# Kernel optimization log

Measured on AMD Instinct MI355X. Metric: run time of the kernel, lower is better.

The kernel has to match this reference:

```python
import jax, jax.numpy as jnp
import numpy as np

MIN_NORM = 1e-15
BALL_EPS = 4e-3  # float32 boundary eps used by the PoincareBall manifold


def _norm(x):
    return jnp.maximum(jnp.linalg.norm(x, axis=-1, keepdims=True), MIN_NORM)


def _artanh(x):
    # clamp like torch Artanh autograd fn (1e-7 margin)
    return jnp.arctanh(jnp.clip(x, -1.0 + 1e-7, 1.0 - 1e-7))


def proj(x, c):
    n = _norm(x)
    maxnorm = (1.0 - BALL_EPS) / jnp.sqrt(c)
    return jnp.where(n > maxnorm, x / n * maxnorm, x)


def expmap0(u, c):
    sc = jnp.sqrt(c)
    n = _norm(u)
    return jnp.tanh(sc * n) * u / (sc * n)


def logmap0(p, c):
    sc = jnp.sqrt(c)
    n = _norm(p)
    return _artanh(sc * n) * p / (sc * n)


def mobius_add(x, y, c):
    x2 = jnp.sum(x * x, axis=-1, keepdims=True)
    y2 = jnp.sum(y * y, axis=-1, keepdims=True)
    xy = jnp.sum(x * y, axis=-1, keepdims=True)
    num = (1.0 + 2.0 * c * xy + c * y2) * x + (1.0 - c * x2) * y
    denom = 1.0 + 2.0 * c * xy + c * c * x2 * y2
    return num / jnp.maximum(denom, MIN_NORM)


def mobius_matvec(m, x, c):
    sc = jnp.sqrt(c)
    xn = _norm(x)
    mx = x @ m.T  # [N, out]
    mxn = _norm(mx)
    res = jnp.tanh(mxn / xn * _artanh(sc * xn)) * mx / (mxn * sc)
    is_zero = jnp.all(mx == 0, axis=-1, keepdims=True)
    return jnp.where(is_zero, jnp.zeros_like(res), res)


def setup_inputs() -> dict:
    key = jax.random.key(0)
    N, D_IN, D_OUT, E = 100000, 128, 128, 1600000
    k1, k2, k3, k4, k5 = jax.random.split(key, 5)
    # points inside the Poincare ball (||x|| ~ 0.34 < 1)
    x = 0.03 * jax.random.normal(k1, (N, D_IN), dtype=jnp.float32)
    # xavier_uniform with gain sqrt(2)
    limit = np.sqrt(2.0) * np.sqrt(6.0 / (D_IN + D_OUT))
    weight = jax.random.uniform(k2, (D_OUT, D_IN), minval=-limit, maxval=limit, dtype=jnp.float32)
    bias = jnp.zeros((D_OUT,), dtype=jnp.float32)
    edge_index = jax.random.randint(k3, (2, E), 0, N, dtype=jnp.int64)
    edge_weight = jax.random.uniform(k4, (E,), dtype=jnp.float32) / 16.0
    return {"x": x, "weight": weight, "bias": bias,
            "edge_index": edge_index, "edge_weight": edge_weight,
            "num_nodes": N}


def reference(x, weight, bias, edge_index, edge_weight, num_nodes):
    c_in = 1.0
    c_out = 1.0
    # --- OriginHypLinear (dropout=0 / eval) ---
    mv = proj(mobius_matvec(weight, x, c_in), c_in)
    hyp_bias = proj(expmap0(bias[None, :], c_in), c_in)  # proj_tan0 is identity
    h = proj(mobius_add(mv, hyp_bias, c_in), c_in)
    # --- OriginHypAgg: logmap0 -> spmm -> expmap0 ---
    xt = logmap0(h, c_in)
    dst, src = edge_index[0], edge_index[1]
    support = jax.ops.segment_sum(edge_weight[:, None] * xt[src], dst,
                                  num_segments=num_nodes)
    h = proj(expmap0(support, c_in), c_in)
    # --- OriginHypAct: relu in tangent space ---
    xt = jax.nn.relu(logmap0(h, c_in))  # proj_tan0 identity
    return proj(expmap0(xt, c_out), c_out)
```

## Files before the change

kernel.cpp:

```cpp
#include <hip/hip_runtime.h>
#include <math.h>

#define D 128
#define MAXNORM 0.996f
#define MINNORM 1e-15f
#define ATCLAMP (1.0f - 1e-7f)

#define CHUNK 2048
#define BSH   7
#define MAXNB 1024
#define SCAP  6144

typedef unsigned int   u32;
typedef unsigned short u16;

typedef __attribute__((ext_vector_type(8))) short bf16x8;
typedef __attribute__((ext_vector_type(4))) float f32x4;

__device__ __forceinline__ float wsum(float v) {
#pragma unroll
  for (int m = 32; m; m >>= 1) v += __shfl_xor(v, m);
  return v;
}
__device__ __forceinline__ float rsum16(float v) {
#pragma unroll
  for (int m = 1; m <= 8; m <<= 1) v += __shfl_xor(v, m);
  return v;
}

__device__ __forceinline__ float frcp(float x) { return __builtin_amdgcn_rcpf(x); }

__device__ __forceinline__ float fast_artanh(float x) {
  x = fminf(x, ATCLAMP);
  return 0.5f * __logf((1.0f + x) * frcp(1.0f - x));
}
__device__ __forceinline__ float fast_tanh(float z) {
  float t = __expf(-2.0f * z);
  return (1.0f - t) * frcp(1.0f + t);
}

__device__ __forceinline__ float bflo(u32 u) { return __uint_as_float(u << 16); }
__device__ __forceinline__ float bfhi(u32 u) { return __uint_as_float(u & 0xffff0000u); }
__device__ __forceinline__ u16 f2bf(float f) {
  u32 u = __float_as_uint(f);
  return (u16)((u + 0x7fffu + ((u >> 16) & 1u)) >> 16);
}
__device__ __forceinline__ float bf2f(u16 h) { return __uint_as_float(((u32)h) << 16); }

union U4B8 { uint4 u; bf16x8 b; };
__device__ __forceinline__ bf16x8 as_b8(uint4 v) { U4B8 c; c.u = v; return c.b; }

__device__ __forceinline__ bool detect_bf16(const u32* p) {
  float lo = fabsf(bflo(p[threadIdx.x & 63]));
  return (bool)__all(lo < 1.0f);
}
__device__ __forceinline__ bool detect_i64(const int* p) {
  return (bool)__all(p[2 * (threadIdx.x & 63) + 1] == 0);
}

template<bool BF>
__device__ __forceinline__ void k1_body(const void* xv, const void* Wv,
                                        const void* bv, u16* xt, int N,
                                        uint4* Wh, uint4* Wl) {
  const int tid  = threadIdx.x;
  const int lane = tid & 63;
  const int wid  = tid >> 6;
  const int qg   = lane >> 4;
  const int lc   = lane & 15;

  for (int slot = tid; slot < 2048; slot += 256) {
    const int l = slot & 63, frag = slot >> 6;
    const int t = frag >> 2, ks = frag & 3;
    const int j  = (l & 15) + 16 * t;
    const int k0 = 32 * ks + 8 * (l >> 4);
    if (BF) {
      Wh[slot] = ((const uint4*)Wv)[j * 16 + (k0 >> 3)];
    } else {
      const float* Wf = (const float*)Wv;
      float4 f0 = *(const float4*)(Wf + (size_t)j * D + k0);
      float4 f1 = *(const float4*)(Wf + (size_t)j * D + k0 + 4);
      float f[8] = {f0.x, f0.y, f0.z, f0.w, f1.x, f1.y, f1.z, f1.w};
      u32 hw[4], lw[4];
#pragma unroll
      for (int i = 0; i < 4; ++i) {
        u16 h0 = f2bf(f[2*i]),  h1 = f2bf(f[2*i+1]);
        u16 l0 = f2bf(f[2*i]   - bf2f(h0));
        u16 l1 = f2bf(f[2*i+1] - bf2f(h1));
        hw[i] = (u32)h0 | ((u32)h1 << 16);
        lw[i] = (u32)l0 | ((u32)l1 << 16);
      }
      Wh[slot] = make_uint4(hw[0], hw[1], hw[2], hw[3]);
      Wl[slot] = make_uint4(lw[0], lw[1], lw[2], lw[3]);
    }
  }

  float bfr[8];
  float nb2 = 0.f;
#pragma unroll
  for (int t = 0; t < 8; ++t) {
    float v = BF ? bf2f(((const u16*)bv)[lc + 16 * t])
                 : ((const float*)bv)[lc + 16 * t];
    bfr[t] = v; nb2 += v * v;
  }
  nb2 = rsum16(nb2);
  float y2;
  {
    float nb = fmaxf(sqrtf(nb2), MINNORM);
    float s  = fast_tanh(nb) * frcp(nb);
    float n1 = s * nb;
    if (n1 > MAXNORM) s *= MAXNORM * frcp(n1);
#pragma unroll
    for (int t = 0; t < 8; ++t) bfr[t] *= s;
    y2 = s * s * nb2;
  }
  const bool bias_zero = (y2 == 0.0f);

  __syncthreads();

  const int tile  = blockIdx.x * 4 + wid;
  const int rbase = tile * 16;
  if (rbase >= N) return;

  int rowA = rbase + lc; if (rowA >= N) rowA = N - 1;
  uint4 Ah[4], Al[4];
  float xn2 = 0.f;
  if (BF) {
    const uint4* xr = (const uint4*)((const u16*)xv + (size_t)rowA * D);
#pragma unroll
    for (int ks = 0; ks < 4; ++ks) {
      uint4 v = xr[4 * ks + qg];
      Ah[ks] = v;
      float a0 = bflo(v.x), a1 = bfhi(v.x), a2 = bflo(v.y), a3 = bfhi(v.y);
      float a4 = bflo(v.z), a5 = bfhi(v.z), a6 = bflo(v.w), a7 = bfhi(v.w);
      xn2 += a0*a0 + a1*a1 + a2*a2 + a3*a3 + a4*a4 + a5*a5 + a6*a6 + a7*a7;
    }
  } else {
    const float4* xr = (const float4*)((const float*)xv + (size_t)rowA * D);
#pragma unroll
    for (int ks = 0; ks < 4; ++ks) {
      float4 f0 = xr[8 * ks + 2 * qg], f1 = xr[8 * ks + 2 * qg + 1];
      float f[8] = {f0.x, f0.y, f0.z, f0.w, f1.x, f1.y, f1.z, f1.w};
      u32 hw[4], lw[4];
#pragma unroll
      for (int i = 0; i < 4; ++i) {
        u16 h0 = f2bf(f[2*i]),  h1 = f2bf(f[2*i+1]);
        u16 l0 = f2bf(f[2*i]   - bf2f(h0));
        u16 l1 = f2bf(f[2*i+1] - bf2f(h1));
        hw[i] = (u32)h0 | ((u32)h1 << 16);
        lw[i] = (u32)l0 | ((u32)l1 << 16);
        xn2 += f[2*i] * f[2*i] + f[2*i+1] * f[2*i+1];
      }
      Ah[ks] = make_uint4(hw[0], hw[1], hw[2], hw[3]);
      Al[ks] = make_uint4(lw[0], lw[1], lw[2], lw[3]);
    }
  }
  xn2 += __shfl_xor(xn2, 16);
  xn2 += __shfl_xor(xn2, 32);

  f32x4 acc[8];
  const f32x4 zero = {0.f, 0.f, 0.f, 0.f};
#pragma unroll
  for (int t = 0; t < 8; ++t) acc[t] = zero;
#pragma unroll
  for (int ks = 0; ks < 4; ++ks) {
    bf16x8 a = as_b8(Ah[ks]);
    bf16x8 al;
    if (!BF) al = as_b8(Al[ks]);
#pragma unroll
    for (int t = 0; t < 8; ++t) {
      const int idx = (t * 4 + ks) * 64 + lane;
      bf16x8 bh = as_b8(Wh[idx]);
      acc[t] = __builtin_amdgcn_mfma_f32_16x16x32_bf16(a, bh, acc[t], 0, 0, 0);
      if (!BF) {
        bf16x8 bl = as_b8(Wl[idx]);
        acc[t] = __builtin_amdgcn_mfma_f32_16x16x32_bf16(al, bh, acc[t], 0, 0, 0);
        acc[t] = __builtin_amdgcn_mfma_f32_16x16x32_bf16(a,  bl, acc[t], 0, 0, 0);
      }
    }
  }

#pragma unroll
  for (int q = 0; q < 4; ++q) {
    const int row_off = qg * 4 + q;
    const int row = rbase + row_off;
    float xnq = fmaxf(sqrtf(__shfl(xn2, row_off)), MINNORM);
    float s2 = 0.f;
#pragma unroll
    for (int t = 0; t < 8; ++t) { float v = acc[t][q]; s2 += v * v; }
    s2 = rsum16(s2);
    float mxn = fmaxf(sqrtf(s2), MINNORM);
    float r = fast_tanh(mxn * frcp(xnq) * fast_artanh(xnq)) * frcp(mxn);
    float pn = r * mxn;
    if (pn > MAXNORM) { r *= MAXNORM * frcp(pn); pn = MAXNORM; }
    float h[8];
    float hn;
    if (bias_zero) {
#pragma unroll
      for (int t = 0; t < 8; ++t) h[t] = r * acc[t][q];
      hn = pn;
    } else {
      float xy = 0.f;
#pragma unroll
      for (int t = 0; t < 8; ++t) { h[t] = r * acc[t][q]; xy += h[t] * bfr[t]; }
      xy = rsum16(xy);
      float x2 = pn * pn;
      float ca = 1.f + 2.f * xy + y2;
      float cb = 1.f - x2;
      float id = frcp(fmaxf(1.f + 2.f * xy + x2 * y2, MINNORM));
      float s3 = 0.f;
#pragma unroll
      for (int t = 0; t < 8; ++t) { h[t] = (ca * h[t] + cb * bfr[t]) * id; s3 += h[t] * h[t]; }
      hn = fmaxf(sqrtf(rsum16(s3)), MINNORM);
    }
    float ps = (hn > MAXNORM) ? (MAXNORM * frcp(hn)) : 1.f;
    float np = fmaxf(hn * ps, MINNORM);
    float tsc = fast_artanh(np) * frcp(np) * ps;
    if (row < N) {
      u16* xo = xt + (size_t)row * D + lc;
#pragma unroll
      for (int t = 0; t < 8; ++t) xo[16 * t] = f2bf(tsc * h[t]);
    }
  }
}

extern "C" __global__ __launch_bounds__(256)
void OriginHyperbolicGraphConvolution_38628935860614_kernel(
    const void* x, const void* W, const void* b, u16* xt, int N) {
  __shared__ uint4 Wh[2048];
  __shared__ uint4 Wl[2048];
  if (detect_bf16((const u32*)x)) k1_body<true >(x, W, b, xt, N, Wh, Wl);
  else                            k1_body<false>(x, W, b, xt, N, Wh, Wl);
}

extern "C" __global__ __launch_bounds__(256) void ksA(
    const int* ei, const void* ew, uint2* ebuck, u16* soffs, int E, int N, int nb) {
  __shared__ int   hist[MAXNB];
  __shared__ int   sArr[MAXNB + 1];
  __shared__ int   psum[256];
  __shared__ uint2 recs[CHUNK];
  const bool i64 = detect_i64(ei);
  const bool bf  = detect_bf16((const u32*)ew);
  const int tid   = threadIdx.x;
  const int cbase = blockIdx.x * CHUNK;

  for (int i = tid; i < MAXNB; i += 256) hist[i] = 0;
  __syncthreads();

  int bkt[8], rank[8]; u32 px[8], wb[8]; bool val[8];
#pragma unroll
  for (int r = 0; r < 8; ++r) {
    const int e = cbase + r * 256 + tid;
    val[r] = false;
    if (e < E) {
      int dst, src;
      if (i64) { dst = ei[2 * (size_t)e]; src = ei[2 * ((size_t)E + e)]; }
      else     { dst = ei[e];             src = ei[(size_t)E + e]; }
      if ((unsigned)dst < (unsigned)N && (unsigned)src < (unsigned)N) {
        val[r] = true;
        bkt[r] = dst >> BSH;
        px[r]  = (u32)src | ((u32)(dst & ((1 << BSH) - 1)) << 17);
        float w;
        if (bf) w = bf2f(((const u16*)ew)[e]); else w = ((const float*)ew)[e];
        wb[r] = __float_as_uint(w);
        rank[r] = atomicAdd(&hist[bkt[r]], 1);
      }
    }
  }
  __syncthreads();

  const int g0 = tid * 4;
  int loc[4], ts = 0;
#pragma unroll
  for (int i = 0; i < 4; ++i) { loc[i] = ts; ts += hist[g0 + i]; }
  psum[tid] = ts; __syncthreads();
#pragma unroll
  for (int off = 1; off < 256; off <<= 1) {
    int t = (tid >= off) ? psum[tid - off] : 0;
    __syncthreads();
    psum[tid] += t;
    __syncthreads();
  }
  const int excl = psum[tid] - ts;
#pragma unroll
  for (int i = 0; i < 4; ++i) sArr[g0 + i] = excl + loc[i];
  if (tid == 255) sArr[MAXNB] = psum[255];
  __syncthreads();

#pragma unroll
  for (int r = 0; r < 8; ++r) if (val[r])
    recs[sArr[bkt[r]] + rank[r]] = make_uint2(px[r], wb[r]);
  __syncthreads();

  const int vcnt = sArr[MAXNB];
  for (int i = tid; i < vcnt; i += 256) ebuck[(size_t)cbase + i] = recs[i];
  u16* so = soffs + (size_t)blockIdx.x * (nb + 1);
  for (int b = tid; b <= nb; b += 256) so[b] = (u16)sArr[b];
}

extern "C" __global__ __launch_bounds__(256) void ks2sum(
    const u16* soffs, int* btot, int nb, int nchunks) {
  __shared__ int red[256];
  const int b = blockIdx.x, tid = threadIdx.x;
  int s = 0;
  for (int c = tid; c < nchunks; c += 256) {
    const u16* so = soffs + (size_t)c * (nb + 1) + b;
    s += (int)so[1] - (int)so[0];
  }
  red[tid] = s; __syncthreads();
#pragma unroll
  for (int off = 128; off; off >>= 1) {
    if (tid < off) red[tid] += red[tid + off];
    __syncthreads();
  }
  if (tid == 0) btot[b] = red[0];
}

extern "C" __global__ __launch_bounds__(1024) void ks2scan(
    const int* btot, int* bbase, int nb) {
  __shared__ int sc[1024];
  const int t = threadIdx.x;
  int v = (t < nb) ? btot[t] : 0;
  sc[t] = v; __syncthreads();
#pragma unroll
  for (int off = 1; off < 1024; off <<= 1) {
    int u = (t >= off) ? sc[t - off] : 0;
    __syncthreads();
    sc[t] += u;
    __syncthreads();
  }
  if (t < nb) bbase[t] = sc[t] - v;
  if (t == 1023) bbase[nb] = sc[1023];
}

extern "C" __global__ __launch_bounds__(256) void ks3(
    const uint2* ebuck, const u16* soffs, const int* bbase,
    uint2* esrt, int* offs, int N, int nb, int nchunks) {
  __shared__ uint2 stage[SCAP];
  __shared__ int hist[128], sc[128], cur[128];
  __shared__ int lcur;
  const int tid = threadIdx.x;
  const int b = blockIdx.x;
  const int s0 = bbase[b], s1 = bbase[b + 1], sz = s1 - s0;
  if (tid < 128) hist[tid] = 0;
  if (tid == 0) lcur = 0;
  __syncthreads();

  const bool fit = (sz <= SCAP);
  if (fit) {
    for (int c = tid; c < nchunks; c += 256) {
      const u16* so = soffs + (size_t)c * (nb + 1) + b;
      const int a = so[0], e = so[1];
      if (e > a) {
        const int base = atomicAdd(&lcur, e - a);
        for (int j = a; j < e; ++j) {
          const uint2 r = ebuck[(size_t)c * CHUNK + j];
          stage[base + (j - a)] = r;
          atomicAdd(&hist[(r.x >> 17) & 127], 1);
        }
      }
    }
  } else {
    for (int c = tid; c < nchunks; c += 256) {
      const u16* so = soffs + (size_t)c * (nb + 1) + b;
      for (int j = so[0]; j < so[1]; ++j)
        atomicAdd(&hist[(ebuck[(size_t)c * CHUNK + j].x >> 17) & 127], 1);
    }
  }
  __syncthreads();

  int v = 0;
  if (tid < 128) { v = hist[tid]; sc[tid] = v; }
  __syncthreads();
#pragma unroll
  for (int off = 1; off < 128; off <<= 1) {
    int t = (tid < 128 && tid >= off) ? sc[tid - off] : 0;
    __syncthreads();
    if (tid < 128) sc[tid] += t;
    __syncthreads();
  }
  if (tid < 128) {
    const int st = sc[tid] - v;
    cur[tid] = st;
    const int node = (b << BSH) + tid;
    if (node < N) offs[node] = s0 + st;
  }
  if (tid == 0 && b == nb - 1) offs[N] = s1;
  __syncthreads();

  if (fit) {
    for (int i = tid; i < sz; i += 256) {
      const uint2 r = stage[i];
      const int d = atomicAdd(&cur[(r.x >> 17) & 127], 1);
      esrt[s0 + d] = make_uint2(r.x & 0x1FFFFu, r.y);
    }
  } else {
    for (int c = tid; c < nchunks; c += 256) {
      const u16* so = soffs + (size_t)c * (nb + 1) + b;
      for (int j = so[0]; j < so[1]; ++j) {
        const uint2 r = ebuck[(size_t)c * CHUNK + j];
        const int d = atomicAdd(&cur[(r.x >> 17) & 127], 1);
        esrt[s0 + d] = make_uint2(r.x & 0x1FFFFu, r.y);
      }
    }
  }
}

extern "C" __global__ __launch_bounds__(256) void kagg(
    const int* offs, const uint2* esrt, const u16* xt,
    void* out, const void* xdet, int N) {
  const bool bf = detect_bf16((const u32*)xdet);
  const int lane = threadIdx.x & 63;
  const int node = blockIdx.x * 4 + (threadIdx.x >> 6);
  if (node >= N) return;
  int s0 = __builtin_amdgcn_readfirstlane(offs[node]);
  int s1 = __builtin_amdgcn_readfirstlane(offs[node + 1]);
  const uint2* ep = esrt + s0;
  const int cnt = s1 - s0;
  const u32* xtw = (const u32*)xt;
  float a0 = 0.f, a1 = 0.f;
  int i = 0;
  for (; i + 8 <= cnt; i += 8) {
    uint2 e[8]; u32 u[8];
#pragma unroll
    for (int k = 0; k < 8; ++k) e[k] = ep[i + k];
#pragma unroll
    for (int k = 0; k < 8; ++k) u[k] = xtw[(e[k].x << 6) | lane];
#pragma unroll
    for (int k = 0; k < 8; ++k) {
      const float w = __uint_as_float(e[k].y);
      a0 += w * bflo(u[k]);
      a1 += w * bfhi(u[k]);
    }
  }
  for (; i + 4 <= cnt; i += 4) {
    uint2 e[4]; u32 u[4];
#pragma unroll
    for (int k = 0; k < 4; ++k) e[k] = ep[i + k];
#pragma unroll
    for (int k = 0; k < 4; ++k) u[k] = xtw[(e[k].x << 6) | lane];
#pragma unroll
    for (int k = 0; k < 4; ++k) {
      const float w = __uint_as_float(e[k].y);
      a0 += w * bflo(u[k]);
      a1 += w * bfhi(u[k]);
    }
  }
  for (; i < cnt; ++i) {
    const uint2 e = ep[i];
    const u32 u = xtw[(e.x << 6) | lane];
    const float w = __uint_as_float(e.y);
    a0 += w * bflo(u);
    a1 += w * bfhi(u);
  }
  float n = fmaxf(sqrtf(wsum(a0 * a0 + a1 * a1)), MINNORM);
  float tn = fast_tanh(n);
  float m = tn * frcp(n);
  if (tn > MAXNORM) { m *= MAXNORM * frcp(tn); tn = MAXNORM; }
  float nn = fmaxf(tn, MINNORM);
  m *= fast_artanh(nn) * frcp(nn);
  float tA = fmaxf(m * a0, 0.f), tB = fmaxf(m * a1, 0.f);
  float nr = fmaxf(sqrtf(wsum(tA * tA + tB * tB)), MINNORM);
  float t2 = fast_tanh(nr);
  float m2 = t2 * frcp(nr);
  if (t2 > MAXNORM) m2 *= MAXNORM * frcp(t2);
  float oA = m2 * tA, oB = m2 * tB;
  if (bf) {
    u32 o = ((u32)f2bf(oA)) | (((u32)f2bf(oB)) << 16);
    ((u32*)out)[(size_t)node * 64 + lane] = o;
  } else {
    ((float2*)out)[(size_t)node * 64 + lane] = make_float2(oA, oB);
  }
}

extern "C" void kernel_launch(void* const* d_in, const int* in_sizes, int n_in,
                              void* d_out, int out_size, void* d_ws, size_t ws_size,
                              hipStream_t stream) {
  const void* x    = d_in[0];
  const void* W    = d_in[1];
  const void* bias = d_in[2];
  const int*  ei   = (const int*)d_in[3];
  const void* ew   = d_in[4];
  const int N = in_sizes[0] / D;
  const int E = in_sizes[4];
  const int nchunks = (E + CHUNK - 1) / CHUNK;
  const int nb      = (N + (1 << BSH) - 1) >> BSH;

  char* ws = (char*)d_ws;
  size_t off = 0;
  auto carve = [&](size_t bytes) { char* p = ws + off; off = (off + bytes + 255) & ~(size_t)255; return p; };
  u16*   xt     = (u16*)  carve((size_t)N * D * sizeof(u16));
  uint2* ebuck  = (uint2*)carve((size_t)nchunks * CHUNK * sizeof(uint2));
  uint2* esrt   = (uint2*)carve((size_t)E * sizeof(uint2));
  u16*   soffs  = (u16*)  carve((size_t)nchunks * (nb + 1) * sizeof(u16));
  int*   btot   = (int*)  carve((size_t)nb * sizeof(int));
  int*   bbase  = (int*)  carve((size_t)(nb + 1) * sizeof(int));
  int*   offs   = (int*)  carve((size_t)(N + 1) * sizeof(int));

  OriginHyperbolicGraphConvolution_38628935860614_kernel<<<(N + 63) / 64, 256, 0, stream>>>(
      x, W, bias, xt, N);
  ksA   <<<nchunks, 256, 0, stream>>>(ei, ew, ebuck, soffs, E, N, nb);
  ks2sum<<<nb, 256, 0, stream>>>(soffs, btot, nb, nchunks);
  ks2scan<<<1, 1024, 0, stream>>>(btot, bbase, nb);
  ks3   <<<nb, 256, 0, stream>>>(ebuck, soffs, bbase, esrt, offs, N, nb, nchunks);
  kagg  <<<(N + 3) / 4, 256, 0, stream>>>(offs, esrt, xt, d_out, x, N);
}
```

Before: 271.4 us.

## Switch GEMM to single fp16 MFMA, fuse bucket scans, persist tiles, widen gather

The split-bf16 three-MFMA product is replaced by a single fp16 MFMA, and the intermediate tangent features are stored as fp16. The two scan kernels are removed: bucket totals are accumulated atomically in ksA, and each ks3 block computes its own prefix, with offsets stored as (start,count) pairs. The linear kernel becomes a persistent grid-stride loop with occupancy hints and also zeroes the counters. The aggregation loop is unrolled to 16 edges. Together these cut launches, LDS use and MFMA work, at the cost of fp16 range and precision risk and a redundant per-block prefix sum.

Measured after the change: 310.8 us. 1.15x slower.

```diff
diff --git a/kernel.cpp b/kernel.cpp
--- a/kernel.cpp
+++ b/kernel.cpp
@@ -9,12 +9,13 @@
 #define CHUNK 2048
 #define BSH   7
 #define MAXNB 1024
-#define SCAP  6144
+#define SCAP2 5120
 
 typedef unsigned int   u32;
 typedef unsigned short u16;
 
-typedef __attribute__((ext_vector_type(8))) short bf16x8;
+typedef __attribute__((ext_vector_type(8))) _Float16 f16x8;
+typedef __attribute__((ext_vector_type(2))) __fp16   h2raw;
 typedef __attribute__((ext_vector_type(4))) float f32x4;
 
 __device__ __forceinline__ float wsum(float v) {
@@ -41,14 +42,18 @@
 
 __device__ __forceinline__ float bflo(u32 u) { return __uint_as_float(u << 16); }
 __device__ __forceinline__ float bfhi(u32 u) { return __uint_as_float(u & 0xffff0000u); }
-__device__ __forceinline__ u16 f2bf(float f) {
-  u32 u = __float_as_uint(f);
-  return (u16)((u + 0x7fffu + ((u >> 16) & 1u)) >> 16);
-}
 __device__ __forceinline__ float bf2f(u16 h) { return __uint_as_float(((u32)h) << 16); }
 
-union U4B8 { uint4 u; bf16x8 b; };
-__device__ __forceinline__ bf16x8 as_b8(uint4 v) { U4B8 c; c.u = v; return c.b; }
+union H2U { h2raw h; u32 u; };
+__device__ __forceinline__ u32 pkh(float a, float b) {
+  H2U c; c.h = __builtin_amdgcn_cvt_pkrtz(a, b); return c.u;
+}
+union U2H { u32 u; _Float16 h[2]; };
+union U4H8 { uint4 u; f16x8 h; };
+__device__ __forceinline__ f16x8 as_h8(uint4 v) { U4H8 c; c.u = v; return c.h; }
+__device__ __forceinline__ u16 f2h(float f) {
+  _Float16 h = (_Float16)f; return *(u16*)&h;
+}
 
 __device__ __forceinline__ bool detect_bf16(const u32* p) {
   float lo = fabsf(bflo(p[threadIdx.x & 63]));
@@ -61,7 +66,7 @@
 template<bool BF>
 __device__ __forceinline__ void k1_body(const void* xv, const void* Wv,
                                         const void* bv, u16* xt, int N,
-                                        uint4* Wh, uint4* Wl) {
+                                        uint4* Wh) {
   const int tid  = threadIdx.x;
   const int lane = tid & 63;
   const int wid  = tid >> 6;
@@ -73,25 +78,20 @@
     const int t = frag >> 2, ks = frag & 3;
     const int j  = (l & 15) + 16 * t;
     const int k0 = 32 * ks + 8 * (l >> 4);
+    float f[8];
     if (BF) {
-      Wh[slot] = ((const uint4*)Wv)[j * 16 + (k0 >> 3)];
+      uint4 v = ((const uint4*)Wv)[j * 16 + (k0 >> 3)];
+      f[0] = bflo(v.x); f[1] = bfhi(v.x); f[2] = bflo(v.y); f[3] = bfhi(v.y);
+      f[4] = bflo(v.z); f[5] = bfhi(v.z); f[6] = bflo(v.w); f[7] = bfhi(v.w);
     } else {
       const float* Wf = (const float*)Wv;
       float4 f0 = *(const float4*)(Wf + (size_t)j * D + k0);
       float4 f1 = *(const float4*)(Wf + (size_t)j * D + k0 + 4);
-      float f[8] = {f0.x, f0.y, f0.z, f0.w, f1.x, f1.y, f1.z, f1.w};
-      u32 hw[4], lw[4];
-#pragma unroll
-      for (int i = 0; i < 4; ++i) {
-        u16 h0 = f2bf(f[2*i]),  h1 = f2bf(f[2*i+1]);
-        u16 l0 = f2bf(f[2*i]   - bf2f(h0));
-        u16 l1 = f2bf(f[2*i+1] - bf2f(h1));
-        hw[i] = (u32)h0 | ((u32)h1 << 16);
-        lw[i] = (u32)l0 | ((u32)l1 << 16);
-      }
-      Wh[slot] = make_uint4(hw[0], hw[1], hw[2], hw[3]);
-      Wl[slot] = make_uint4(lw[0], lw[1], lw[2], lw[3]);
-    }
+      f[0]=f0.x; f[1]=f0.y; f[2]=f0.z; f[3]=f0.w;
+      f[4]=f1.x; f[5]=f1.y; f[6]=f1.z; f[7]=f1.w;
+    }
+    Wh[slot] = make_uint4(pkh(f[0],f[1]), pkh(f[2],f[3]),
+                          pkh(f[4],f[5]), pkh(f[6],f[7]));
   }
 
   float bfr[8];
@@ -117,123 +117,105 @@
 
   __syncthreads();
 
-  const int tile  = blockIdx.x * 4 + wid;
-  const int rbase = tile * 16;
-  if (rbase >= N) return;
-
-  int rowA = rbase + lc; if (rowA >= N) rowA = N - 1;
-  uint4 Ah[4], Al[4];
-  float xn2 = 0.f;
-  if (BF) {
-    const uint4* xr = (const uint4*)((const u16*)xv + (size_t)rowA * D);
+  const int T = (N + 15) >> 4;
+  for (int tile = blockIdx.x * 4 + wid; tile < T; tile += gridDim.x * 4) {
+    const int rbase = tile * 16;
+    int rowA = rbase + lc; if (rowA >= N) rowA = N - 1;
+    uint4 Ah[4];
+    float xn2 = 0.f;
 #pragma unroll
     for (int ks = 0; ks < 4; ++ks) {
-      uint4 v = xr[4 * ks + qg];
-      Ah[ks] = v;
-      float a0 = bflo(v.x), a1 = bfhi(v.x), a2 = bflo(v.y), a3 = bfhi(v.y);
-      float a4 = bflo(v.z), a5 = bfhi(v.z), a6 = bflo(v.w), a7 = bfhi(v.w);
-      xn2 += a0*a0 + a1*a1 + a2*a2 + a3*a3 + a4*a4 + a5*a5 + a6*a6 + a7*a7;
-    }
-  } else {
-    const float4* xr = (const float4*)((const float*)xv + (size_t)rowA * D);
+      float f[8];
+      if (BF) {
+        uint4 v = ((const uint4*)((const u16*)xv + (size_t)rowA * D))[4 * ks + qg];
+        f[0]=bflo(v.x); f[1]=bfhi(v.x); f[2]=bflo(v.y); f[3]=bfhi(v.y);
+        f[4]=bflo(v.z); f[5]=bfhi(v.z); f[6]=bflo(v.w); f[7]=bfhi(v.w);
+      } else {
+        const float4* xr = (const float4*)((const float*)xv + (size_t)rowA * D);
+        float4 f0 = xr[8 * ks + 2 * qg], f1 = xr[8 * ks + 2 * qg + 1];
+        f[0]=f0.x; f[1]=f0.y; f[2]=f0.z; f[3]=f0.w;
+        f[4]=f1.x; f[5]=f1.y; f[6]=f1.z; f[7]=f1.w;
+      }
+#pragma unroll
+      for (int i = 0; i < 8; ++i) xn2 += f[i] * f[i];
+      Ah[ks] = make_uint4(pkh(f[0],f[1]), pkh(f[2],f[3]),
+                          pkh(f[4],f[5]), pkh(f[6],f[7]));
+    }
+    xn2 += __shfl_xor(xn2, 16);
+    xn2 += __shfl_xor(xn2, 32);
+
+    f32x4 acc[8];
+    const f32x4 zero = {0.f, 0.f, 0.f, 0.f};
+#pragma unroll
+    for (int t = 0; t < 8; ++t) acc[t] = zero;
 #pragma unroll
     for (int ks = 0; ks < 4; ++ks) {
-      float4 f0 = xr[8 * ks + 2 * qg], f1 = xr[8 * ks + 2 * qg + 1];
-      float f[8] = {f0.x, f0.y, f0.z, f0.w, f1.x, f1.y, f1.z, f1.w};
-      u32 hw[4], lw[4];
-#pragma unroll
-      for (int i = 0; i < 4; ++i) {
-        u16 h0 = f2bf(f[2*i]),  h1 = f2bf(f[2*i+1]);
-        u16 l0 = f2bf(f[2*i]   - bf2f(h0));
-        u16 l1 = f2bf(f[2*i+1] - bf2f(h1));
-        hw[i] = (u32)h0 | ((u32)h1 << 16);
-        lw[i] = (u32)l0 | ((u32)l1 << 16);
-        xn2 += f[2*i] * f[2*i] + f[2*i+1] * f[2*i+1];
-      }
-      Ah[ks] = make_uint4(hw[0], hw[1], hw[2], hw[3]);
-      Al[ks] = make_uint4(lw[0], lw[1], lw[2], lw[3]);
-    }
-  }
-  xn2 += __shfl_xor(xn2, 16);
-  xn2 += __shfl_xor(xn2, 32);
-
-  f32x4 acc[8];
-  const f32x4 zero = {0.f, 0.f, 0.f, 0.f};
-#pragma unroll
-  for (int t = 0; t < 8; ++t) acc[t] = zero;
-#pragma unroll
-  for (int ks = 0; ks < 4; ++ks) {
-    bf16x8 a = as_b8(Ah[ks]);
-    bf16x8 al;
-    if (!BF) al = as_b8(Al[ks]);
-#pragma unroll
-    for (int t = 0; t < 8; ++t) {
-      const int idx = (t * 4 + ks) * 64 + lane;
-      bf16x8 bh = as_b8(Wh[idx]);
-      acc[t] = __builtin_amdgcn_mfma_f32_16x16x32_bf16(a, bh, acc[t], 0, 0, 0);
-      if (!BF) {
-        bf16x8 bl = as_b8(Wl[idx]);
-        acc[t] = __builtin_amdgcn_mfma_f32_16x16x32_bf16(al, bh, acc[t], 0, 0, 0);
-        acc[t] = __builtin_amdgcn_mfma_f32_16x16x32_bf16(a,  bl, acc[t], 0, 0, 0);
-      }
-    }
-  }
-
-#pragma unroll
-  for (int q = 0; q < 4; ++q) {
-    const int row_off = qg * 4 + q;
-    const int row = rbase + row_off;
-    float xnq = fmaxf(sqrtf(__shfl(xn2, row_off)), MINNORM);
-    float s2 = 0.f;
-#pragma unroll
-    for (int t = 0; t < 8; ++t) { float v = acc[t][q]; s2 += v * v; }
-    s2 = rsum16(s2);
-    float mxn = fmaxf(sqrtf(s2), MINNORM);
-    float r = fast_tanh(mxn * frcp(xnq) * fast_artanh(xnq)) * frcp(mxn);
-    float pn = r * mxn;
-    if (pn > MAXNORM) { r *= MAXNORM * frcp(pn); pn = MAXNORM; }
-    float h[8];
-    float hn;
-    if (bias_zero) {
-#pragma unroll
-      for (int t = 0; t < 8; ++t) h[t] = r * acc[t][q];
-      hn = pn;
-    } else {
-      float xy = 0.f;
-#pragma unroll
-      for (int t = 0; t < 8; ++t) { h[t] = r * acc[t][q]; xy += h[t] * bfr[t]; }
-      xy = rsum16(xy);
-      float x2 = pn * pn;
-      float ca = 1.f + 2.f * xy + y2;
-      float cb = 1.f - x2;
-      float id = frcp(fmaxf(1.f + 2.f * xy + x2 * y2, MINNORM));
-      float s3 = 0.f;
-#pragma unroll
-      for (int t = 0; t < 8; ++t) { h[t] = (ca * h[t] + cb * bfr[t]) * id; s3 += h[t] * h[t]; }
-      hn = fmaxf(sqrtf(rsum16(s3)), MINNORM);
-    }
-    float ps = (hn > MAXNORM) ? (MAXNORM * frcp(hn)) : 1.f;
-    float np = fmaxf(hn * ps, MINNORM);
-    float tsc = fast_artanh(np) * frcp(np) * ps;
-    if (row < N) {
-      u16* xo = xt + (size_t)row * D + lc;
-#pragma unroll
-      for (int t = 0; t < 8; ++t) xo[16 * t] = f2bf(tsc * h[t]);
-    }
-  }
-}
-
-extern "C" __global__ __launch_bounds__(256)
+      f16x8 a = as_h8(Ah[ks]);
+#pragma unroll
+      for (int t = 0; t < 8; ++t) {
+        f16x8 bh = as_h8(Wh[(t * 4 + ks) * 64 + lane]);
+        acc[t] = __builtin_amdgcn_mfma_f32_16x16x32_f16(a, bh, acc[t], 0, 0, 0);
+      }
+    }
+
+#pragma unroll
+    for (int q = 0; q < 4; ++q) {
+      const int row_off = qg * 4 + q;
+      const int row = rbase + row_off;
+      float xnq = fmaxf(sqrtf(__shfl(xn2, row_off)), MINNORM);
+      float s2 = 0.f;
+#pragma unroll
+      for (int t = 0; t < 8; ++t) { float v = acc[t][q]; s2 += v * v; }
+      s2 = rsum16(s2);
+      float mxn = fmaxf(sqrtf(s2), MINNORM);
+      float r = fast_tanh(mxn * frcp(xnq) * fast_artanh(xnq)) * frcp(mxn);
+      float pn = r * mxn;
+      if (pn > MAXNORM) { r *= MAXNORM * frcp(pn); pn = MAXNORM; }
+      float h[8];
+      float hn;
+      if (bias_zero) {
+#pragma unroll
+        for (int t = 0; t < 8; ++t) h[t] = r * acc[t][q];
+        hn = pn;
+      } else {
+        float xy = 0.f;
+#pragma unroll
+        for (int t = 0; t < 8; ++t) { h[t] = r * acc[t][q]; xy += h[t] * bfr[t]; }
+        xy = rsum16(xy);
+        float x2 = pn * pn;
+        float ca = 1.f + 2.f * xy + y2;
+        float cb = 1.f - x2;
+        float id = frcp(fmaxf(1.f + 2.f * xy + x2 * y2, MINNORM));
+        float s3 = 0.f;
+#pragma unroll
+        for (int t = 0; t < 8; ++t) { h[t] = (ca * h[t] + cb * bfr[t]) * id; s3 += h[t] * h[t]; }
+        hn = fmaxf(sqrtf(rsum16(s3)), MINNORM);
+      }
+      float ps = (hn > MAXNORM) ? (MAXNORM * frcp(hn)) : 1.f;
+      float np = fmaxf(hn * ps, MINNORM);
+      float tsc = fast_artanh(np) * frcp(np) * ps;
+      if (row < N) {
+        u16* xo = xt + (size_t)row * D + lc;
+#pragma unroll
+        for (int t = 0; t < 8; ++t) xo[16 * t] = f2h(tsc * h[t]);
+      }
+    }
+  }
+}
+
+extern "C" __global__ __launch_bounds__(256, 4)
 void OriginHyperbolicGraphConvolution_38628935860614_kernel(
-    const void* x, const void* W, const void* b, u16* xt, int N) {
+    const void* x, const void* W, const void* b, u16* xt, int* btot, int N) {
   __shared__ uint4 Wh[2048];
-  __shared__ uint4 Wl[2048];
-  if (detect_bf16((const u32*)x)) k1_body<true >(x, W, b, xt, N, Wh, Wl);
-  else                            k1_body<false>(x, W, b, xt, N, Wh, Wl);
+  if (blockIdx.x == 0)
+    for (int i = threadIdx.x; i < MAXNB; i += 256) btot[i] = 0;
+  if (detect_bf16((const u32*)x)) k1_body<true >(x, W, b, xt, N, Wh);
+  else                            k1_body<false>(x, W, b, xt, N, Wh);
 }
 
 extern "C" __global__ __launch_bounds__(256) void ksA(
-    const int* ei, const void* ew, uint2* ebuck, u16* soffs, int E, int N, int nb) {
+    const int* ei, const void* ew, uint2* ebuck, u16* soffs, int* btot,
+    int E, int N, int nb) {
   __shared__ int   hist[MAXNB];
   __shared__ int   sArr[MAXNB + 1];
   __shared__ int   psum[256];
@@ -253,8 +235,12 @@
     val[r] = false;
     if (e < E) {
       int dst, src;
-      if (i64) { dst = ei[2 * (size_t)e]; src = ei[2 * ((size_t)E + e)]; }
-      else     { dst = ei[e];             src = ei[(size_t)E + e]; }
+      if (i64) {
+        dst = (int)((const uint2*)ei)[(size_t)e].x;
+        src = (int)((const uint2*)ei)[(size_t)E + e].x;
+      } else {
+        dst = ei[e]; src = ei[(size_t)E + e];
+      }
       if ((unsigned)dst < (unsigned)N && (unsigned)src < (unsigned)N) {
         val[r] = true;
         bkt[r] = dst >> BSH;
@@ -295,57 +281,38 @@
   for (int i = tid; i < vcnt; i += 256) ebuck[(size_t)cbase + i] = recs[i];
   u16* so = soffs + (size_t)blockIdx.x * (nb + 1);
   for (int b = tid; b <= nb; b += 256) so[b] = (u16)sArr[b];
-}
-
-extern "C" __global__ __launch_bounds__(256) void ks2sum(
-    const u16* soffs, int* btot, int nb, int nchunks) {
+  for (int b = tid; b < nb; b += 256) {
+    const int len = sArr[b + 1] - sArr[b];
+    if (len) atomicAdd(&btot[b], len);
+  }
+}
+
+extern "C" __global__ __launch_bounds__(256) void ks3(
+    const uint2* ebuck, const u16* soffs, const int* btot,
+    uint2* esrt, uint2* offs2, int N, int nb, int nchunks) {
+  __shared__ uint2 stage[SCAP2];
   __shared__ int red[256];
-  const int b = blockIdx.x, tid = threadIdx.x;
-  int s = 0;
-  for (int c = tid; c < nchunks; c += 256) {
-    const u16* so = soffs + (size_t)c * (nb + 1) + b;
-    s += (int)so[1] - (int)so[0];
-  }
-  red[tid] = s; __syncthreads();
-#pragma unroll
-  for (int off = 128; off; off >>= 1) {
-    if (tid < off) red[tid] += red[tid + off];
-    __syncthreads();
-  }
-  if (tid == 0) btot[b] = red[0];
-}
-
-extern "C" __global__ __launch_bounds__(1024) void ks2scan(
-    const int* btot, int* bbase, int nb) {
-  __shared__ int sc[1024];
-  const int t = threadIdx.x;
-  int v = (t < nb) ? btot[t] : 0;
-  sc[t] = v; __syncthreads();
-#pragma unroll
-  for (int off = 1; off < 1024; off <<= 1) {
-    int u = (t >= off) ? sc[t - off] : 0;
-    __syncthreads();
-    sc[t] += u;
-    __syncthreads();
-  }
-  if (t < nb) bbase[t] = sc[t] - v;
-  if (t == 1023) bbase[nb] = sc[1023];
-}
-
-extern "C" __global__ __launch_bounds__(256) void ks3(
-    const uint2* ebuck, const u16* soffs, const int* bbase,
-    uint2* esrt, int* offs, int N, int nb, int nchunks) {
-  __shared__ uint2 stage[SCAP];
   __shared__ int hist[128], sc[128], cur[128];
   __shared__ int lcur;
   const int tid = threadIdx.x;
   const int b = blockIdx.x;
-  const int s0 = bbase[b], s1 = bbase[b + 1], sz = s1 - s0;
+
+  int part = 0;
+  for (int i = tid; i < b; i += 256) part += btot[i];
+  red[tid] = part;
   if (tid < 128) hist[tid] = 0;
   if (tid == 0) lcur = 0;
   __syncthreads();
-
-  const bool fit = (sz <= SCAP);
+#pragma unroll
+  for (int off = 128; off; off >>= 1) {
+    if (tid < off) red[tid] += red[tid + off];
+    __syncthreads();
+  }
+  const int s0  = red[0];
+  const int cnt = btot[b];
+  const int node0 = b << BSH;
+
+  const bool fit = (cnt <= SCAP2);
   if (fit) {
     for (int c = tid; c < nchunks; c += 256) {
       const u16* so = soffs + (size_t)c * (nb + 1) + b;
@@ -381,14 +348,13 @@
   if (tid < 128) {
     const int st = sc[tid] - v;
     cur[tid] = st;
-    const int node = (b << BSH) + tid;
-    if (node < N) offs[node] = s0 + st;
-  }
-  if (tid == 0 && b == nb - 1) offs[N] = s1;
+    const int node = node0 + tid;
+    if (node < N) offs2[node] = make_uint2((u32)(s0 + st), (u32)v);
+  }
   __syncthreads();
 
   if (fit) {
-    for (int i = tid; i < sz; i += 256) {
+    for (int i = tid; i < cnt; i += 256) {
       const uint2 r = stage[i];
       const int d = atomicAdd(&cur[(r.x >> 17) & 127], 1);
       esrt[s0 + d] = make_uint2(r.x & 0x1FFFFu, r.y);
@@ -406,30 +372,31 @@
 }
 
 extern "C" __global__ __launch_bounds__(256) void kagg(
-    const int* offs, const uint2* esrt, const u16* xt,
+    const uint2* offs2, const uint2* esrt, const u16* xt,
     void* out, const void* xdet, int N) {
   const bool bf = detect_bf16((const u32*)xdet);
   const int lane = threadIdx.x & 63;
   const int node = blockIdx.x * 4 + (threadIdx.x >> 6);
   if (node >= N) return;
-  int s0 = __builtin_amdgcn_readfirstlane(offs[node]);
-  int s1 = __builtin_amdgcn_readfirstlane(offs[node + 1]);
+  const uint2 oo = offs2[node];
+  const int s0  = __builtin_amdgcn_readfirstlane((int)oo.x);
+  const int cnt = __builtin_amdgcn_readfirstlane((int)oo.y);
   const uint2* ep = esrt + s0;
-  const int cnt = s1 - s0;
   const u32* xtw = (const u32*)xt;
   float a0 = 0.f, a1 = 0.f;
   int i = 0;
-  for (; i + 8 <= cnt; i += 8) {
-    uint2 e[8]; u32 u[8];
-#pragma unroll
-    for (int k = 0; k < 8; ++k) e[k] = ep[i + k];
-#pragma unroll
-    for (int k = 0; k < 8; ++k) u[k] = xtw[(e[k].x << 6) | lane];
-#pragma unroll
-    for (int k = 0; k < 8; ++k) {
+  for (; i + 16 <= cnt; i += 16) {
+    uint2 e[16]; u32 u[16];
+#pragma unroll
+    for (int k = 0; k < 16; ++k) e[k] = ep[i + k];
+#pragma unroll
+    for (int k = 0; k < 16; ++k) u[k] = xtw[(e[k].x << 6) | lane];
+#pragma unroll
+    for (int k = 0; k < 16; ++k) {
       const float w = __uint_as_float(e[k].y);
-      a0 += w * bflo(u[k]);
-      a1 += w * bfhi(u[k]);
+      U2H c; c.u = u[k];
+      a0 += w * (float)c.h[0];
+      a1 += w * (float)c.h[1];
     }
   }
   for (; i + 4 <= cnt; i += 4) {
@@ -441,16 +408,18 @@
 #pragma unroll
     for (int k = 0; k < 4; ++k) {
       const float w = __uint_as_float(e[k].y);
-      a0 += w * bflo(u[k]);
-      a1 += w * bfhi(u[k]);
+      U2H c; c.u = u[k];
+      a0 += w * (float)c.h[0];
+      a1 += w * (float)c.h[1];
     }
   }
   for (; i < cnt; ++i) {
     const uint2 e = ep[i];
     const u32 u = xtw[(e.x << 6) | lane];
     const float w = __uint_as_float(e.y);
-    a0 += w * bflo(u);
-    a1 += w * bfhi(u);
+    U2H c; c.u = u;
+    a0 += w * (float)c.h[0];
+    a1 += w * (float)c.h[1];
   }
   float n = fmaxf(sqrtf(wsum(a0 * a0 + a1 * a1)), MINNORM);
   float tn = fast_tanh(n);
@@ -465,8 +434,10 @@
   if (t2 > MAXNORM) m2 *= MAXNORM * frcp(t2);
   float oA = m2 * tA, oB = m2 * tB;
   if (bf) {
-    u32 o = ((u32)f2bf(oA)) | (((u32)f2bf(oB)) << 16);
-    ((u32*)out)[(size_t)node * 64 + lane] = o;
+    u32 ua = __float_as_uint(oA), ub = __float_as_uint(oB);
+    u32 ra = (ua + 0x7fffu + ((ua >> 16) & 1u)) >> 16;
+    u32 rb = (ub + 0x7fffu + ((ub >> 16) & 1u)) >> 16;
+    ((u32*)out)[(size_t)node * 64 + lane] = ra | (rb << 16);
   } else {
     ((float2*)out)[(size_t)node * 64 + lane] = make_float2(oA, oB);
   }
@@ -488,19 +459,19 @@
   char* ws = (char*)d_ws;
   size_t off = 0;
   auto carve = [&](size_t bytes) { char* p = ws + off; off = (off + bytes + 255) & ~(size_t)255; return p; };
-  u16*   xt     = (u16*)  carve((size_t)N * D * sizeof(u16));
-  uint2* ebuck  = (uint2*)carve((size_t)nchunks * CHUNK * sizeof(uint2));
-  uint2* esrt   = (uint2*)carve((size_t)E * sizeof(uint2));
-  u16*   soffs  = (u16*)  carve((size_t)nchunks * (nb + 1) * sizeof(u16));
-  int*   btot   = (int*)  carve((size_t)nb * sizeof(int));
-  int*   bbase  = (int*)  carve((size_t)(nb + 1) * sizeof(int));
-  int*   offs   = (int*)  carve((size_t)(N + 1) * sizeof(int));
-
-  OriginHyperbolicGraphConvolution_38628935860614_kernel<<<(N + 63) / 64, 256, 0, stream>>>(
-      x, W, bias, xt, N);
-  ksA   <<<nchunks, 256, 0, stream>>>(ei, ew, ebuck, soffs, E, N, nb);
-  ks2sum<<<nb, 256, 0, stream>>>(soffs, btot, nb, nchunks);
-  ks2scan<<<1, 1024, 0, stream>>>(btot, bbase, nb);
-  ks3   <<<nb, 256, 0, stream>>>(ebuck, soffs, bbase, esrt, offs, N, nb, nchunks);
-  kagg  <<<(N + 3) / 4, 256, 0, stream>>>(offs, esrt, xt, d_out, x, N);
-}
+  u16*   xt    = (u16*)  carve((size_t)N * D * sizeof(u16));
+  uint2* ebuck = (uint2*)carve((size_t)nchunks * CHUNK * sizeof(uint2));
+  uint2* esrt  = (uint2*)carve((size_t)E * sizeof(uint2));
+  u16*   soffs = (u16*)  carve((size_t)nchunks * (nb + 1) * sizeof(u16));
+  uint2* offs2 = (uint2*)carve((size_t)N * sizeof(uint2));
+  int*   btot  = (int*)  carve((size_t)MAXNB * sizeof(int));
+
+  const int T  = (N + 15) / 16;
+  const int g1 = min((T + 3) / 4, 1024);
+
+  OriginHyperbolicGraphConvolution_38628935860614_kernel<<<g1, 256, 0, stream>>>(
+      x, W, bias, xt, btot, N);
+  ksA <<<nchunks, 256, 0, stream>>>(ei, ew, ebuck, soffs, btot, E, N, nb);
+  ks3 <<<nb, 256, 0, stream>>>(ebuck, soffs, btot, esrt, offs2, N, nb, nchunks);
+  kagg<<<(N + 3) / 4, 256, 0, stream>>>(offs2, esrt, xt, d_out, x, N);
+}
```
